# Kernel tuning notes

Hardware: AMD Instinct MI355X
Metric: run time of the kernel (lower is better)

Reference implementation:

```python
import jax, jax.numpy as jnp
import numpy as np

TEMPERATURE = 0.07
EPS = 1e-06


def setup_inputs() -> dict:
    key = jax.random.key(0)
    k1, k2 = jax.random.split(key)
    feats = jax.random.normal(k1, (8192, 512), dtype=jnp.float32)
    # module expects L2-normalized features
    feats = feats / jnp.linalg.norm(feats, axis=1, keepdims=True)
    labels = jax.random.randint(k2, (8192,), 0, 100, dtype=jnp.int64 if jax.config.jax_enable_x64 else jnp.int32)
    return {"features": feats, "labels": labels}


def reference(features, labels):
    n = features.shape[0]
    sim = jnp.matmul(features, features.T)                      # [N, N]
    lab = labels.reshape(-1, 1)
    mask = (lab == lab.T).astype(features.dtype)                # same-class mask
    logits_mask = 1.0 - jnp.eye(n, dtype=features.dtype)        # exclude self
    mask = mask * logits_mask
    logits = sim / TEMPERATURE
    logits_max = jax.lax.stop_gradient(jnp.max(logits, axis=1, keepdims=True))
    logits = logits - logits_max
    exp_logits = jnp.exp(logits) * logits_mask
    log_prob = logits - jnp.log(jnp.sum(exp_logits, axis=1, keepdims=True) + EPS)
    mean_log_prob_pos = jnp.sum(mask * log_prob, axis=1) / (jnp.sum(mask, axis=1) + EPS)
    return -jnp.mean(mean_log_prob_pos)
```

## Files before the change

kernel.cpp:

```cpp
#include <hip/hip_runtime.h>

#define NN 8192
#define KK 512
#define INVT 14.285714285714286f
#define K2E 20.60992915555662f
#define EPSF 1e-6f

#define BM 128
#define BN 64
#define CSPLIT 8
#define COLS_PER_BLOCK (NN / CSPLIT)
#define NTILES (COLS_PER_BLOCK / BN)

typedef short bf16x8 __attribute__((ext_vector_type(8)));
typedef float f32x4 __attribute__((ext_vector_type(4)));

__device__ __forceinline__ unsigned short f2bf(float f) {
  unsigned int u = __float_as_uint(f);
  u = u + 0x7FFFu + ((u >> 16) & 1u);
  return (unsigned short)(u >> 16);
}

__device__ __forceinline__ void load_lds16(const void* g, void* l) {
  __builtin_amdgcn_global_load_lds(
      (const __attribute__((address_space(1))) unsigned int*)g,
      (__attribute__((address_space(3))) unsigned int*)l, 16, 0, 0);
}

__global__ void prep_kernel(const float* __restrict__ feats,
                            const int* __restrict__ labels,
                            unsigned short* __restrict__ fb,
                            int* __restrict__ cnt) {
  int tid = blockIdx.x * 256 + threadIdx.x;
  const float4* src = (const float4*)feats + (size_t)tid * 2;
  float4 a = src[0];
  float4 b = src[1];
  bf16x8 o;
  o[0] = (short)f2bf(a.x); o[1] = (short)f2bf(a.y);
  o[2] = (short)f2bf(a.z); o[3] = (short)f2bf(a.w);
  o[4] = (short)f2bf(b.x); o[5] = (short)f2bf(b.y);
  o[6] = (short)f2bf(b.z); o[7] = (short)f2bf(b.w);
  *(bf16x8*)(fb + (size_t)tid * 8) = o;
  if (tid < NN) atomicAdd(&cnt[labels[tid]], 1);
}

__global__ __launch_bounds__(256, 2) void
scl_main_kernel(const unsigned short* __restrict__ fb,
                const int* __restrict__ labels,
                float* __restrict__ Sarr, float* __restrict__ Parr) {
  __shared__ unsigned short lds[BN * KK];

  const int bid = blockIdx.x;
  const int rowTile = bid / CSPLIT;
  const int colChunk = bid % CSPLIT;
  const bool diagBlk = ((rowTile >> 3) == colChunk);
  const int tid = threadIdx.x;
  const int w = tid >> 6;
  const int l = tid & 63;
  const int lo = l & 15;
  const int g = l >> 4;

  const int row0 = rowTile * BM + w * 32;
  const int myrow0 = row0 + g * 4;
  const int myrow1 = row0 + 16 + g * 4;

  bf16x8 Af0[16], Af1[16];
  {
    const unsigned short* a0 = fb + (size_t)(row0 + lo) * KK;
    const unsigned short* a1 = fb + (size_t)(row0 + 16 + lo) * KK;
#pragma unroll
    for (int ks = 0; ks < 16; ++ks) {
      Af0[ks] = *(const bf16x8*)(a0 + ks * 32 + g * 8);
      Af1[ks] = *(const bf16x8*)(a1 + ks * 32 + g * 8);
    }
  }

  int labr0[4], labr1[4];
#pragma unroll
  for (int r = 0; r < 4; ++r) {
    labr0[r] = labels[myrow0 + r];
    labr1[r] = labels[myrow1 + r];
  }

  f32x4 Sac0 = {0.f,0.f,0.f,0.f}, Sac1 = {0.f,0.f,0.f,0.f};
  f32x4 Pac0 = {0.f,0.f,0.f,0.f}, Pac1 = {0.f,0.f,0.f,0.f};

  const int colbase0 = colChunk * COLS_PER_BLOCK;

  for (int t = 0; t < NTILES; ++t) {
    const int colbase = colbase0 + t * BN;
    __syncthreads();
#pragma unroll
    for (int j = 0; j < 16; ++j) {
      const int col = w * 16 + j;
      const int kc = (l & 56) | ((l ^ col) & 7);
      const unsigned short* src = fb + (size_t)(colbase + col) * KK + kc * 8;
      load_lds16((const void*)src, (void*)&lds[col * KK]);
    }
    __syncthreads();

#pragma unroll
    for (int st = 0; st < 4; ++st) {
      const int ct = st * 16 + lo;
      const int colg = colbase + ct;
      const int labc = labels[colg];
      f32x4 a0 = {0.f,0.f,0.f,0.f};
      f32x4 a1 = {0.f,0.f,0.f,0.f};
#pragma unroll
      for (int ks = 0; ks < 16; ++ks) {
        const int kc = ks * 4 + g;
        const int phys = (kc & 56) | ((kc ^ ct) & 7);
        bf16x8 Bf = *(const bf16x8*)(&lds[ct * KK + phys * 8]);
        a0 = __builtin_amdgcn_mfma_f32_16x16x32_bf16(Af0[ks], Bf, a0, 0, 0, 0);
        a1 = __builtin_amdgcn_mfma_f32_16x16x32_bf16(Af1[ks], Bf, a1, 0, 0, 0);
      }
#pragma unroll
      for (int r = 0; r < 4; ++r) {
        const float s0 = a0[r];
        const float e0 = __builtin_amdgcn_exp2f(__builtin_fmaf(s0, K2E, -K2E));
        Sac0[r] += e0;
        if (labc == labr0[r]) Pac0[r] += s0;
        const float s1 = a1[r];
        const float e1 = __builtin_amdgcn_exp2f(__builtin_fmaf(s1, K2E, -K2E));
        Sac1[r] += e1;
        if (labc == labr1[r]) Pac1[r] += s1;
        if (diagBlk) {
          if (colg == myrow0 + r) { Sac0[r] -= e0; Pac0[r] -= s0; }
          if (colg == myrow1 + r) { Sac1[r] -= e1; Pac1[r] -= s1; }
        }
      }
    }
  }

#pragma unroll
  for (int r = 0; r < 4; ++r) {
    float s0 = Sac0[r], p0 = Pac0[r], s1 = Sac1[r], p1 = Pac1[r];
#pragma unroll
    for (int m = 1; m < 16; m <<= 1) {
      s0 += __shfl_xor(s0, m, 64);
      p0 += __shfl_xor(p0, m, 64);
      s1 += __shfl_xor(s1, m, 64);
      p1 += __shfl_xor(p1, m, 64);
    }
    if (lo == 0) {
      atomicAdd(&Sarr[myrow0 + r], s0);
      atomicAdd(&Parr[myrow0 + r], p0);
      atomicAdd(&Sarr[myrow1 + r], s1);
      atomicAdd(&Parr[myrow1 + r], p1);
    }
  }
}

__global__ void finish_kernel(const float* __restrict__ Sarr,
                              const float* __restrict__ Parr,
                              const int* __restrict__ labels,
                              const int* __restrict__ cnt,
                              float* __restrict__ out) {
  int i = blockIdx.x * 256 + threadIdx.x;
  float v = 0.f;
  if (i < NN) {
    float C = (float)(cnt[labels[i]] - 1);
    float lp = Parr[i] * INVT - C * (INVT + logf(Sarr[i] + EPSF));
    v = lp / (C + EPSF);
  }
#pragma unroll
  for (int m = 1; m < 64; m <<= 1) v += __shfl_xor(v, m, 64);
  if ((threadIdx.x & 63) == 0) atomicAdd(out, -v * (1.0f / NN));
}

extern "C" void kernel_launch(void* const* d_in, const int* in_sizes, int n_in,
                              void* d_out, int out_size, void* d_ws, size_t ws_size,
                              hipStream_t stream) {
  const float* feats = (const float*)d_in[0];
  const int* labels = (const int*)d_in[1];

  unsigned short* fb = (unsigned short*)d_ws;
  const size_t FB_BYTES = (size_t)NN * KK * 2;
  float* Sarr = (float*)((char*)d_ws + FB_BYTES);
  float* Parr = Sarr + NN;
  int* cnt = (int*)(Parr + NN);

  hipMemsetAsync((char*)d_ws + FB_BYTES, 0, (size_t)NN * 8 + 512, stream);
  hipMemsetAsync(d_out, 0, sizeof(float), stream);

  prep_kernel<<<dim3((NN * KK / 8) / 256), dim3(256), 0, stream>>>(feats, labels, fb, cnt);
  scl_main_kernel<<<dim3(64 * CSPLIT), dim3(256), 0, stream>>>(fb, labels, Sarr, Parr);
  finish_kernel<<<dim3(NN / 256), dim3(256), 0, stream>>>(Sarr, Parr, labels, cnt, (float*)d_out);
}
```

Measured before the change: 99.34 us.

## Exploit symmetry of similarity matrix by computing only upper-triangle tiles

The grid now covers only the upper-triangular 128x128 block pairs of the symmetric Gram matrix, and each off-diagonal tile also adds its column sums (exp and positive-sim) into the column rows via atomics. This roughly halves the MFMA work and the B-tile loads. In exchange it adds many more atomics per block (one pair per 16 columns per wave), a loop decoding the triangular index, and smaller blocks (2 column halves) with less reuse of the A fragments loaded from global memory.

After: 121.2 us. +22.0%, slower.

```diff
diff --git a/kernel.cpp b/kernel.cpp
--- a/kernel.cpp
+++ b/kernel.cpp
@@ -6,11 +6,8 @@
 #define K2E 20.60992915555662f
 #define EPSF 1e-6f
 
-#define BM 128
-#define BN 64
-#define CSPLIT 8
-#define COLS_PER_BLOCK (NN / CSPLIT)
-#define NTILES (COLS_PER_BLOCK / BN)
+#define NB 64
+#define NTRI (NB * (NB + 1) / 2)
 
 typedef short bf16x8 __attribute__((ext_vector_type(8)));
 typedef float f32x4 __attribute__((ext_vector_type(4)));
@@ -48,19 +45,21 @@
 scl_main_kernel(const unsigned short* __restrict__ fb,
                 const int* __restrict__ labels,
                 float* __restrict__ Sarr, float* __restrict__ Parr) {
-  __shared__ unsigned short lds[BN * KK];
-
-  const int bid = blockIdx.x;
-  const int rowTile = bid / CSPLIT;
-  const int colChunk = bid % CSPLIT;
-  const bool diagBlk = ((rowTile >> 3) == colChunk);
+  __shared__ unsigned short lds[64 * KK];
+
+  int rb = 0, rem = blockIdx.x;
+  while (rem >= NB - rb) { rem -= NB - rb; ++rb; }
+  const int cb = rb + rem;
+  const bool diag = (rb == cb);
+
   const int tid = threadIdx.x;
   const int w = tid >> 6;
   const int l = tid & 63;
   const int lo = l & 15;
   const int g = l >> 4;
 
-  const int row0 = rowTile * BM + w * 32;
+  const int row0 = rb * 128 + w * 32;
+  const int colBase = cb * 128;
   const int myrow0 = row0 + g * 4;
   const int myrow1 = row0 + 16 + g * 4;
 
@@ -81,20 +80,25 @@
     labr0[r] = labels[myrow0 + r];
     labr1[r] = labels[myrow1 + r];
   }
+  int labc[2][4];
+#pragma unroll
+  for (int h = 0; h < 2; ++h)
+#pragma unroll
+    for (int st = 0; st < 4; ++st)
+      labc[h][st] = labels[colBase + h * 64 + st * 16 + lo];
 
   f32x4 Sac0 = {0.f,0.f,0.f,0.f}, Sac1 = {0.f,0.f,0.f,0.f};
   f32x4 Pac0 = {0.f,0.f,0.f,0.f}, Pac1 = {0.f,0.f,0.f,0.f};
 
-  const int colbase0 = colChunk * COLS_PER_BLOCK;
-
-  for (int t = 0; t < NTILES; ++t) {
-    const int colbase = colbase0 + t * BN;
+#pragma unroll
+  for (int h = 0; h < 2; ++h) {
+    const int colb = colBase + h * 64;
     __syncthreads();
 #pragma unroll
     for (int j = 0; j < 16; ++j) {
       const int col = w * 16 + j;
       const int kc = (l & 56) | ((l ^ col) & 7);
-      const unsigned short* src = fb + (size_t)(colbase + col) * KK + kc * 8;
+      const unsigned short* src = fb + (size_t)(colb + col) * KK + kc * 8;
       load_lds16((const void*)src, (void*)&lds[col * KK]);
     }
     __syncthreads();
@@ -102,8 +106,8 @@
 #pragma unroll
     for (int st = 0; st < 4; ++st) {
       const int ct = st * 16 + lo;
-      const int colg = colbase + ct;
-      const int labc = labels[colg];
+      const int colg = colb + ct;
+      const int lc = labc[h][st];
       f32x4 a0 = {0.f,0.f,0.f,0.f};
       f32x4 a1 = {0.f,0.f,0.f,0.f};
 #pragma unroll
@@ -114,19 +118,32 @@
         a0 = __builtin_amdgcn_mfma_f32_16x16x32_bf16(Af0[ks], Bf, a0, 0, 0, 0);
         a1 = __builtin_amdgcn_mfma_f32_16x16x32_bf16(Af1[ks], Bf, a1, 0, 0, 0);
       }
+      float ce = 0.f, cp = 0.f;
 #pragma unroll
       for (int r = 0; r < 4; ++r) {
         const float s0 = a0[r];
         const float e0 = __builtin_amdgcn_exp2f(__builtin_fmaf(s0, K2E, -K2E));
         Sac0[r] += e0;
-        if (labc == labr0[r]) Pac0[r] += s0;
+        ce += e0;
+        if (lc == labr0[r]) { Pac0[r] += s0; cp += s0; }
         const float s1 = a1[r];
         const float e1 = __builtin_amdgcn_exp2f(__builtin_fmaf(s1, K2E, -K2E));
         Sac1[r] += e1;
-        if (labc == labr1[r]) Pac1[r] += s1;
-        if (diagBlk) {
+        ce += e1;
+        if (lc == labr1[r]) { Pac1[r] += s1; cp += s1; }
+        if (diag) {
           if (colg == myrow0 + r) { Sac0[r] -= e0; Pac0[r] -= s0; }
           if (colg == myrow1 + r) { Sac1[r] -= e1; Pac1[r] -= s1; }
+        }
+      }
+      if (!diag) {
+        ce += __shfl_xor(ce, 16, 64);
+        ce += __shfl_xor(ce, 32, 64);
+        cp += __shfl_xor(cp, 16, 64);
+        cp += __shfl_xor(cp, 32, 64);
+        if (l < 16) {
+          atomicAdd(&Sarr[colg], ce);
+          atomicAdd(&Parr[colg], cp);
         }
       }
     }
@@ -184,6 +201,6 @@
   hipMemsetAsync(d_out, 0, sizeof(float), stream);
 
   prep_kernel<<<dim3((NN * KK / 8) / 256), dim3(256), 0, stream>>>(feats, labels, fb, cnt);
-  scl_main_kernel<<<dim3(64 * CSPLIT), dim3(256), 0, stream>>>(fb, labels, Sarr, Parr);
+  scl_main_kernel<<<dim3(NTRI), dim3(256), 0, stream>>>(fb, labels, Sarr, Parr);
   finish_kernel<<<dim3(NN / 256), dim3(256), 0, stream>>>(Sarr, Parr, labels, cnt, (float*)d_out);
 }
```
